# Performance work log

Measured on AMD Instinct MI355X. Metric: run time of the kernel, lower is better.

## Reference

```python
import jax, jax.numpy as jnp
import numpy as np

B, S, D, E = 4, 4096, 1024, 8

def setup_inputs() -> dict:
    key = jax.random.key(0)
    k1, k2, k3, k4, k5 = jax.random.split(key, 5)
    scale = 1.0 / np.sqrt(D)
    return {
        "x": jax.random.normal(k1, (B, S, D), dtype=jnp.float32),
        "Wg": jax.random.normal(k2, (D, D), dtype=jnp.float32) * scale,   # gate Linear(D, D)
        "bg": jnp.zeros((D,), dtype=jnp.float32),
        "We": jax.random.normal(k3, (E, D, D), dtype=jnp.float32) * scale,  # per-expert Linear(D, D)
        "be": jnp.zeros((E, D), dtype=jnp.float32),
    }

def reference(x, Wg, bg, We, be):
    # gating network: Linear + Softmax over last dim (size D, per the original module)
    probs = jax.nn.softmax(x @ Wg + bg, axis=-1)           # [B,S,D]
    idx = jnp.argmax(probs, axis=-1)                        # [B,S], values in [0, D)
    p = jnp.take_along_axis(probs, idx[..., None], axis=-1)[..., 0]  # top-1 gate prob
    e_idx = idx % We.shape[0]                               # map argmax to expert id
    # run every expert densely, then select routed expert per token (top-1 switch routing)
    h = jax.nn.relu(jnp.einsum('bsd,edf->besf', x, We) + be[None, :, None, :])  # [B,E,S,D]
    onehot = jax.nn.one_hot(e_idx, We.shape[0], dtype=x.dtype)                   # [B,S,E]
    out = jnp.einsum('besf,bse->bsf', h, onehot) * p[..., None]                  # [B,S,D]
    return out
```

## Files before the change

### kernel.cpp

```cpp
#include <hip/hip_runtime.h>
#include <stdint.h>
#include <stddef.h>

#define TOK    16384
#define DDIM   1024
#define NEXP   8
#define BMT    128
#define RB_MAX 136
#define MARGIN 2.5e-2f
#define AMBIG_CAP 4096
#define BK     64

typedef __bf16 bf16x8 __attribute__((ext_vector_type(8)));
typedef float  f32x4  __attribute__((ext_vector_type(4)));
typedef unsigned short u16x8 __attribute__((ext_vector_type(8)));

__device__ __forceinline__ unsigned short f2bf(float f) {
    unsigned int u = __float_as_uint(f);
    u += 0x7fff + ((u >> 16) & 1);
    return (unsigned short)(u >> 16);
}

__device__ __forceinline__ void gload_lds16(const void* g, void* l) {
    __builtin_amdgcn_global_load_lds(
        (const __attribute__((address_space(1))) unsigned int*)g,
        (__attribute__((address_space(3))) unsigned int*)l, 16, 0, 0);
}

__device__ __forceinline__ void seg_starts(const int* __restrict__ cnt, int* st) {
    int total = 0;
#pragma unroll
    for (int e = 0; e < NEXP; e++) {
        st[e] = total;
        total += ((cnt[e] + BMT - 1) / BMT) * BMT;
    }
    st[NEXP] = total;
}

__global__ __launch_bounds__(256) void cvt_x_init(
    const float* __restrict__ x, unsigned short* __restrict__ xbf,
    int* __restrict__ cnt, int* __restrict__ cursor,
    int* __restrict__ n_ambig, int* __restrict__ row_of_slot)
{
    if (blockIdx.x == 0) {
        for (int i = threadIdx.x; i < RB_MAX * BMT; i += 256) row_of_slot[i] = -1;
        if (threadIdx.x < NEXP) { cnt[threadIdx.x] = 0; cursor[threadIdx.x] = 0; }
        if (threadIdx.x == 0) *n_ambig = 0;
    }
    const size_t t = ((size_t)blockIdx.x * 256 + threadIdx.x) * 8;
    const float4 v0 = *(const float4*)(x + t);
    const float4 v1 = *(const float4*)(x + t + 4);
    const float vv[8] = {v0.x, v0.y, v0.z, v0.w, v1.x, v1.y, v1.z, v1.w};
    u16x8 hh;
#pragma unroll
    for (int j = 0; j < 8; j++) hh[j] = f2bf(vv[j]);
    *(u16x8*)(xbf + t) = hh;
}

__global__ __launch_bounds__(256) void transpose_mat(
    const float* __restrict__ src0, unsigned short* __restrict__ dst0)
{
    __shared__ float tile[32][33];
    const int e  = blockIdx.z;
    const int k0 = blockIdx.x * 32;
    const int n0 = blockIdx.y * 32;
    const int tx = threadIdx.x;
    const int ty = threadIdx.y;
    const float* src = src0 + (size_t)e * DDIM * DDIM;
    unsigned short* dst = dst0 + (size_t)e * DDIM * DDIM;
#pragma unroll
    for (int r = 0; r < 4; r++)
        tile[ty + r * 8][tx] = src[(size_t)(k0 + ty + r * 8) * DDIM + n0 + tx];
    __syncthreads();
#pragma unroll
    for (int r = 0; r < 4; r++)
        dst[(size_t)(n0 + ty + r * 8) * DDIM + k0 + tx] = f2bf(tile[tx][ty + r * 8]);
}

__global__ __launch_bounds__(256) void transpose_wg(
    const float* __restrict__ src, unsigned short* __restrict__ dstb,
    float* __restrict__ dstf)
{
    __shared__ float tile[32][33];
    const int k0 = blockIdx.x * 32;
    const int n0 = blockIdx.y * 32;
    const int tx = threadIdx.x;
    const int ty = threadIdx.y;
#pragma unroll
    for (int r = 0; r < 4; r++)
        tile[ty + r * 8][tx] = src[(size_t)(k0 + ty + r * 8) * DDIM + n0 + tx];
    __syncthreads();
#pragma unroll
    for (int r = 0; r < 4; r++) {
        const float v = tile[tx][ty + r * 8];
        const size_t o = (size_t)(n0 + ty + r * 8) * DDIM + k0 + tx;
        dstb[o] = f2bf(v);
        dstf[o] = v;
    }
}

__global__ __launch_bounds__(256) void gating_mfma(
    const unsigned short* __restrict__ xbf,
    const unsigned short* __restrict__ WgT,
    const float* __restrict__ bg, float* __restrict__ logits)
{
    __shared__ unsigned short Asm[128 * BK];
    __shared__ unsigned short Bsm[128 * BK];
    const int rb = blockIdx.x;
    const int nb = blockIdx.y;
    const int tid  = threadIdx.x;
    const int lane = tid & 63;
    const int wave = tid >> 6;
    const int q    = lane >> 4;
    const int m16  = lane & 15;
    const int wrow = (wave & 1) * 64;
    const int wcol = (wave >> 1) * 64;

    const unsigned short* Ag = xbf + (size_t)rb * 128 * DDIM;
    const unsigned short* Bg = WgT + (size_t)nb * 128 * DDIM;

    const unsigned short* pa[4];
    const unsigned short* pb[4];
#pragma unroll
    for (int i = 0; i < 4; i++) {
        const int idx = tid + i * 256;
        const int r = idx >> 3;
        const int c = idx & 7;
        const int g = (c ^ (r & 7)) * 8;
        pa[i] = Ag + (size_t)r * DDIM + g;
        pb[i] = Bg + (size_t)r * DDIM + g;
    }

    f32x4 acc[4][4];
#pragma unroll
    for (int i = 0; i < 4; i++)
#pragma unroll
        for (int j = 0; j < 4; j++) acc[i][j] = (f32x4){0.f, 0.f, 0.f, 0.f};

    for (int k0 = 0; k0 < DDIM; k0 += BK) {
#pragma unroll
        for (int i = 0; i < 4; i++) {
            gload_lds16(pa[i] + k0, &Asm[(tid + i * 256) * 8]);
            gload_lds16(pb[i] + k0, &Bsm[(tid + i * 256) * 8]);
        }
        __syncthreads();
#pragma unroll
        for (int s = 0; s < 2; s++) {
            const int cs = (((s << 2) + q) ^ (m16 & 7)) << 3;
            bf16x8 af[4], bfr[4];
#pragma unroll
            for (int i = 0; i < 4; i++)
                af[i] = *(const bf16x8*)&Asm[(wrow + i * 16 + m16) * BK + cs];
#pragma unroll
            for (int j = 0; j < 4; j++)
                bfr[j] = *(const bf16x8*)&Bsm[(wcol + j * 16 + m16) * BK + cs];
#pragma unroll
            for (int i = 0; i < 4; i++)
#pragma unroll
                for (int j = 0; j < 4; j++)
                    acc[i][j] = __builtin_amdgcn_mfma_f32_16x16x32_bf16(
                        af[i], bfr[j], acc[i][j], 0, 0, 0);
        }
        __syncthreads();
    }

    float bgv[4];
#pragma unroll
    for (int j = 0; j < 4; j++) bgv[j] = bg[nb * 128 + wcol + j * 16 + m16];
#pragma unroll
    for (int i = 0; i < 4; i++)
#pragma unroll
        for (int r = 0; r < 4; r++) {
            const int row = rb * 128 + wrow + i * 16 + q * 4 + r;
#pragma unroll
            for (int j = 0; j < 4; j++) {
                const int col = nb * 128 + wcol + j * 16 + m16;
                logits[(size_t)row * DDIM + col] = acc[i][j][r] + bgv[j];
            }
        }
}

__global__ __launch_bounds__(256) void row_stats(
    const float* __restrict__ logits, float* __restrict__ pout,
    int* __restrict__ eout, float* __restrict__ rmax_a, float* __restrict__ s_a,
    int* __restrict__ ambig, int* __restrict__ n_ambig)
{
    const int row  = blockIdx.x * 4 + (threadIdx.x >> 6);
    const int lane = threadIdx.x & 63;
    const float* L = logits + (size_t)row * DDIM;
    float vals[16];
#pragma unroll
    for (int i = 0; i < 4; i++)
        *(float4*)&vals[i * 4] = *(const float4*)&L[lane * 16 + i * 4];
    float m = vals[0]; int mi = lane * 16;
#pragma unroll
    for (int i = 1; i < 16; i++)
        if (vals[i] > m) { m = vals[i]; mi = lane * 16 + i; }
    for (int off = 32; off > 0; off >>= 1) {
        float ov = __shfl_down(m, off, 64);
        int   oi = __shfl_down(mi, off, 64);
        if (ov > m || (ov == m && oi < mi)) { m = ov; mi = oi; }
    }
    m  = __shfl(m, 0, 64);
    mi = __shfl(mi, 0, 64);
    float s = 0.f;
    int   c = 0;
#pragma unroll
    for (int i = 0; i < 16; i++) {
        s += expf(vals[i] - m);
        if (vals[i] >= m - MARGIN) c++;
    }
    for (int off = 32; off > 0; off >>= 1) {
        s += __shfl_xor(s, off, 64);
        c += __shfl_xor(c, off, 64);
    }
    if (lane == 0) {
        pout[row] = 1.0f / s;
        eout[row] = mi & (NEXP - 1);
        rmax_a[row] = m;
        s_a[row] = s;
        if (c > 1) {
            int k = atomicAdd(n_ambig, 1);
            if (k < AMBIG_CAP) ambig[k] = row;
        }
    }
}

__global__ __launch_bounds__(64) void fixup(
    const float* __restrict__ logits, const float* __restrict__ x,
    const float* __restrict__ WgTf, const float* __restrict__ bg,
    const float* __restrict__ rmax_a, const float* __restrict__ s_a,
    const int* __restrict__ ambig, const int* __restrict__ n_ambig,
    int* __restrict__ eout, float* __restrict__ pout)
{
    int n = *n_ambig; if (n > AMBIG_CAP) n = AMBIG_CAP;
    if ((int)blockIdx.x >= n) return;
    const int row  = ambig[blockIdx.x];
    const int lane = threadIdx.x;
    const float rmax = rmax_a[row];
    const float* L = logits + (size_t)row * DDIM;
    __shared__ int scnt;
    __shared__ int scol[32];
    if (lane == 0) scnt = 0;
    __syncthreads();
    for (int j = lane; j < DDIM; j += 64)
        if (L[j] >= rmax - MARGIN) {
            int k = atomicAdd(&scnt, 1);
            if (k < 32) scol[k] = j;
        }
    __syncthreads();
    int ncand = scnt < 32 ? scnt : 32;
    double bestv = -1e300; int bestc = DDIM;
    for (int cidx = 0; cidx < ncand; cidx++) {
        const int col = scol[cidx];
        const float* Wcol = WgTf + (size_t)col * DDIM;
        double s = 0.0;
        for (int k = lane; k < DDIM; k += 64)
            s += (double)x[(size_t)row * DDIM + k] * (double)Wcol[k];
        for (int off = 32; off > 0; off >>= 1) s += __shfl_down(s, off, 64);
        s = __shfl(s, 0, 64);
        s += (double)bg[col];
        if (s > bestv || (s == bestv && col < bestc)) { bestv = s; bestc = col; }
    }
    if (lane == 0) {
        eout[row] = bestc & (NEXP - 1);
        pout[row] = expf(L[bestc] - rmax) / s_a[row];
    }
}

__global__ __launch_bounds__(256) void histo(const int* __restrict__ eout,
                                             int* __restrict__ cnt)
{
    __shared__ int h[NEXP];
    if (threadIdx.x < NEXP) h[threadIdx.x] = 0;
    __syncthreads();
    const int t = blockIdx.x * 256 + threadIdx.x;
    if (t < TOK) atomicAdd(&h[eout[t]], 1);
    __syncthreads();
    if (threadIdx.x < NEXP) atomicAdd(&cnt[threadIdx.x], h[threadIdx.x]);
}

__global__ __launch_bounds__(256) void assign_slots(
    const int* __restrict__ eout, const int* __restrict__ cnt,
    int* __restrict__ cursor, int* __restrict__ row_of_slot)
{
    __shared__ int h[NEXP];
    __shared__ int base[NEXP];
    __shared__ int sstart[NEXP];
    const int tid = threadIdx.x;
    if (tid < NEXP) {
        h[tid] = 0;
        int st[NEXP + 1];
        seg_starts(cnt, st);
        sstart[tid] = st[tid];
    }
    __syncthreads();
    const int t = blockIdx.x * 256 + tid;
    int e = 0, lr = 0;
    if (t < TOK) {
        e = eout[t];
        lr = atomicAdd(&h[e], 1);
    }
    __syncthreads();
    if (tid < NEXP && h[tid] > 0)
        base[tid] = atomicAdd(&cursor[tid], h[tid]);
    __syncthreads();
    if (t < TOK)
        row_of_slot[sstart[e] + base[e] + lr] = t;
}

__global__ __launch_bounds__(256) void expert_gemm(
    const unsigned short* __restrict__ xbf, const unsigned short* __restrict__ WeT,
    const float* __restrict__ be, const float* __restrict__ p,
    const int* __restrict__ row_of_slot, const int* __restrict__ cnt,
    float* __restrict__ out)
{
    __shared__ unsigned short Asm[128 * BK];
    __shared__ unsigned short Bsm[128 * BK];
    __shared__ int rs[128];
    const int rb = blockIdx.x;
    const int nb = blockIdx.y;

    int st[NEXP + 1];
    seg_starts(cnt, st);
    const int s0 = rb * BMT;
    int e = -1;
#pragma unroll
    for (int ei = 0; ei < NEXP; ei++)
        if (s0 >= st[ei] && s0 < st[ei + 1]) e = ei;
    if (e < 0) return;

    const int tid  = threadIdx.x;
    const int lane = tid & 63;
    const int wave = tid >> 6;
    const int q    = lane >> 4;
    const int m16  = lane & 15;
    const int wrow = (wave & 1) * 64;
    const int wcol = (wave >> 1) * 64;

    if (tid < 128) rs[tid] = row_of_slot[rb * 128 + tid];
    __syncthreads();

    const unsigned short* Bglob = WeT + (size_t)e * DDIM * DDIM + (size_t)nb * 128 * DDIM;

    const unsigned short* pa[4];
    const unsigned short* pb[4];
#pragma unroll
    for (int i = 0; i < 4; i++) {
        const int idx = tid + i * 256;
        const int r = idx >> 3;
        const int c = idx & 7;
        const int g = (c ^ (r & 7)) * 8;
        int tr = rs[r]; if (tr < 0) tr = 0;
        pa[i] = xbf + (size_t)tr * DDIM + g;
        pb[i] = Bglob + (size_t)r * DDIM + g;
    }

    f32x4 acc[4][4];
#pragma unroll
    for (int i = 0; i < 4; i++)
#pragma unroll
        for (int j = 0; j < 4; j++) acc[i][j] = (f32x4){0.f, 0.f, 0.f, 0.f};

    for (int k0 = 0; k0 < DDIM; k0 += BK) {
#pragma unroll
        for (int i = 0; i < 4; i++) {
            gload_lds16(pa[i] + k0, &Asm[(tid + i * 256) * 8]);
            gload_lds16(pb[i] + k0, &Bsm[(tid + i * 256) * 8]);
        }
        __syncthreads();
#pragma unroll
        for (int s = 0; s < 2; s++) {
            const int cs = (((s << 2) + q) ^ (m16 & 7)) << 3;
            bf16x8 af[4], bfr[4];
#pragma unroll
            for (int i = 0; i < 4; i++)
                af[i] = *(const bf16x8*)&Asm[(wrow + i * 16 + m16) * BK + cs];
#pragma unroll
            for (int j = 0; j < 4; j++)
                bfr[j] = *(const bf16x8*)&Bsm[(wcol + j * 16 + m16) * BK + cs];
#pragma unroll
            for (int i = 0; i < 4; i++)
#pragma unroll
                for (int j = 0; j < 4; j++)
                    acc[i][j] = __builtin_amdgcn_mfma_f32_16x16x32_bf16(
                        af[i], bfr[j], acc[i][j], 0, 0, 0);
        }
        __syncthreads();
    }

    float bev[4];
#pragma unroll
    for (int j = 0; j < 4; j++) bev[j] = be[e * DDIM + nb * 128 + wcol + j * 16 + m16];
#pragma unroll
    for (int i = 0; i < 4; i++)
#pragma unroll
        for (int r = 0; r < 4; r++) {
            const int t = rs[wrow + i * 16 + q * 4 + r];
            if (t < 0) continue;
            const float pv = p[t];
#pragma unroll
            for (int j = 0; j < 4; j++) {
                const int n = nb * 128 + wcol + j * 16 + m16;
                float v = acc[i][j][r] + bev[j];
                v = v > 0.f ? v : 0.f;
                out[(size_t)t * DDIM + n] = v * pv;
            }
        }
}

extern "C" void kernel_launch(void* const* d_in, const int* in_sizes, int n_in,
                              void* d_out, int out_size, void* d_ws, size_t ws_size,
                              hipStream_t stream)
{
    const float* x  = (const float*)d_in[0];
    const float* Wg = (const float*)d_in[1];
    const float* bg = (const float*)d_in[2];
    const float* We = (const float*)d_in[3];
    const float* be = (const float*)d_in[4];
    float* out = (float*)d_out;

    char* ws = (char*)d_ws;
    float* logits = (float*)ws;                 ws += (size_t)TOK * DDIM * 4;
    unsigned short* WeT = (unsigned short*)ws;  ws += (size_t)NEXP * DDIM * DDIM * 2;
    unsigned short* WgT = (unsigned short*)ws;  ws += (size_t)DDIM * DDIM * 2;
    float* WgTf = (float*)ws;                   ws += (size_t)DDIM * DDIM * 4;
    unsigned short* xbf = (unsigned short*)ws;  ws += (size_t)TOK * DDIM * 2;
    float* p = (float*)ws;                      ws += (size_t)TOK * 4;
    int* e_arr = (int*)ws;                      ws += (size_t)TOK * 4;
    float* rmax_a = (float*)ws;                 ws += (size_t)TOK * 4;
    float* s_a = (float*)ws;                    ws += (size_t)TOK * 4;
    int* row_of_slot = (int*)ws;                ws += (size_t)RB_MAX * BMT * 4;
    int* cnt = (int*)ws;                        ws += NEXP * 4;
    int* cursor = (int*)ws;                     ws += NEXP * 4;
    int* ambig = (int*)ws;                      ws += AMBIG_CAP * 4;
    int* n_ambig = (int*)ws;                    ws += 4;

    cvt_x_init<<<TOK * DDIM / (256 * 8), 256, 0, stream>>>(
        x, xbf, cnt, cursor, n_ambig, row_of_slot);
    transpose_wg<<<dim3(32, 32), dim3(32, 8), 0, stream>>>(Wg, WgT, WgTf);
    transpose_mat<<<dim3(32, 32, NEXP), dim3(32, 8), 0, stream>>>(We, WeT);
    gating_mfma<<<dim3(TOK / 128, DDIM / 128), 256, 0, stream>>>(xbf, WgT, bg, logits);
    row_stats<<<TOK / 4, 256, 0, stream>>>(logits, p, e_arr, rmax_a, s_a, ambig, n_ambig);
    fixup<<<AMBIG_CAP, 64, 0, stream>>>(logits, x, WgTf, bg, rmax_a, s_a, ambig, n_ambig, e_arr, p);
    histo<<<TOK / 256, 256, 0, stream>>>(e_arr, cnt);
    assign_slots<<<TOK / 256, 256, 0, stream>>>(e_arr, cnt, cursor, row_of_slot);
    expert_gemm<<<dim3(RB_MAX, DDIM / 128), 256, 0, stream>>>(
        xbf, WeT, be, p, row_of_slot, cnt, out);
}
```

Measured before the change: 313.2 us.

## Fuse ambiguity fixup and histogram into row_stats; remap GEMM blocks per XCD

Folds the fp64 recheck of near-tie rows and the per-expert histogram into row_stats, which removes the fixup and histo launches along with the ambiguous-row list. Both GEMMs now use a 1D grid whose block index is remapped so that neighbouring row/column tiles land on the same XCD, aiming for better L2 reuse. The cost is that row_stats waves with ambiguous rows now run the fp64 dot products inline, which can stall their blocks.

After: 323.6 us. 3.3% more time.

```diff
diff --git a/kernel.cpp b/kernel.cpp
--- a/kernel.cpp
+++ b/kernel.cpp
@@ -8,7 +8,6 @@
 #define BMT    128
 #define RB_MAX 136
 #define MARGIN 2.5e-2f
-#define AMBIG_CAP 4096
 #define BK     64
 
 typedef __bf16 bf16x8 __attribute__((ext_vector_type(8)));
@@ -40,12 +39,11 @@
 __global__ __launch_bounds__(256) void cvt_x_init(
     const float* __restrict__ x, unsigned short* __restrict__ xbf,
     int* __restrict__ cnt, int* __restrict__ cursor,
-    int* __restrict__ n_ambig, int* __restrict__ row_of_slot)
+    int* __restrict__ row_of_slot)
 {
     if (blockIdx.x == 0) {
         for (int i = threadIdx.x; i < RB_MAX * BMT; i += 256) row_of_slot[i] = -1;
         if (threadIdx.x < NEXP) { cnt[threadIdx.x] = 0; cursor[threadIdx.x] = 0; }
-        if (threadIdx.x == 0) *n_ambig = 0;
     }
     const size_t t = ((size_t)blockIdx.x * 256 + threadIdx.x) * 8;
     const float4 v0 = *(const float4*)(x + t);
@@ -106,8 +104,13 @@
 {
     __shared__ unsigned short Asm[128 * BK];
     __shared__ unsigned short Bsm[128 * BK];
-    const int rb = blockIdx.x;
-    const int nb = blockIdx.y;
+    const int bid = blockIdx.x;
+    const int xcd = bid & 7;
+    const int seq = bid >> 3;
+    const int cl  = seq >> 6;
+    const int w   = seq & 63;
+    const int rb  = xcd * 16 + (w >> 2);
+    const int nb  = cl * 4 + (w & 3);
     const int tid  = threadIdx.x;
     const int lane = tid & 63;
     const int wave = tid >> 6;
@@ -181,12 +184,20 @@
 }
 
 __global__ __launch_bounds__(256) void row_stats(
-    const float* __restrict__ logits, float* __restrict__ pout,
-    int* __restrict__ eout, float* __restrict__ rmax_a, float* __restrict__ s_a,
-    int* __restrict__ ambig, int* __restrict__ n_ambig)
-{
-    const int row  = blockIdx.x * 4 + (threadIdx.x >> 6);
+    const float* __restrict__ logits, const float* __restrict__ x,
+    const float* __restrict__ WgTf, const float* __restrict__ bg,
+    float* __restrict__ pout, int* __restrict__ eout, int* __restrict__ cnt)
+{
+    __shared__ int   scnt[4];
+    __shared__ int   scol[4][32];
+    __shared__ float sval[4][32];
+    __shared__ int   hcnt[NEXP];
+    const int wv   = threadIdx.x >> 6;
+    const int row  = blockIdx.x * 4 + wv;
     const int lane = threadIdx.x & 63;
+    if (threadIdx.x < NEXP) hcnt[threadIdx.x] = 0;
+    __syncthreads();
+
     const float* L = logits + (size_t)row * DDIM;
     float vals[16];
 #pragma unroll
@@ -214,70 +225,45 @@
         s += __shfl_xor(s, off, 64);
         c += __shfl_xor(c, off, 64);
     }
+
+    int my_e; float my_p;
+    if (c > 1) {
+        if (lane == 0) scnt[wv] = 0;
+#pragma unroll
+        for (int i = 0; i < 16; i++)
+            if (vals[i] >= m - MARGIN) {
+                int k = atomicAdd(&scnt[wv], 1);
+                if (k < 32) { scol[wv][k] = lane * 16 + i; sval[wv][k] = vals[i]; }
+            }
+        int ncand = scnt[wv]; if (ncand > 32) ncand = 32;
+        double bestv = -1e300; int bestc = DDIM; float bestL = 0.f;
+        for (int cidx = 0; cidx < ncand; cidx++) {
+            const int col = scol[wv][cidx];
+            const float* Wcol = WgTf + (size_t)col * DDIM;
+            double sd = 0.0;
+            for (int k = lane; k < DDIM; k += 64)
+                sd += (double)x[(size_t)row * DDIM + k] * (double)Wcol[k];
+            for (int off = 32; off > 0; off >>= 1) sd += __shfl_down(sd, off, 64);
+            sd = __shfl(sd, 0, 64);
+            sd += (double)bg[col];
+            if (sd > bestv || (sd == bestv && col < bestc)) {
+                bestv = sd; bestc = col; bestL = sval[wv][cidx];
+            }
+        }
+        my_e = bestc & (NEXP - 1);
+        my_p = expf(bestL - m) / s;
+    } else {
+        my_e = mi & (NEXP - 1);
+        my_p = 1.0f / s;
+    }
     if (lane == 0) {
-        pout[row] = 1.0f / s;
-        eout[row] = mi & (NEXP - 1);
-        rmax_a[row] = m;
-        s_a[row] = s;
-        if (c > 1) {
-            int k = atomicAdd(n_ambig, 1);
-            if (k < AMBIG_CAP) ambig[k] = row;
-        }
-    }
-}
-
-__global__ __launch_bounds__(64) void fixup(
-    const float* __restrict__ logits, const float* __restrict__ x,
-    const float* __restrict__ WgTf, const float* __restrict__ bg,
-    const float* __restrict__ rmax_a, const float* __restrict__ s_a,
-    const int* __restrict__ ambig, const int* __restrict__ n_ambig,
-    int* __restrict__ eout, float* __restrict__ pout)
-{
-    int n = *n_ambig; if (n > AMBIG_CAP) n = AMBIG_CAP;
-    if ((int)blockIdx.x >= n) return;
-    const int row  = ambig[blockIdx.x];
-    const int lane = threadIdx.x;
-    const float rmax = rmax_a[row];
-    const float* L = logits + (size_t)row * DDIM;
-    __shared__ int scnt;
-    __shared__ int scol[32];
-    if (lane == 0) scnt = 0;
-    __syncthreads();
-    for (int j = lane; j < DDIM; j += 64)
-        if (L[j] >= rmax - MARGIN) {
-            int k = atomicAdd(&scnt, 1);
-            if (k < 32) scol[k] = j;
-        }
-    __syncthreads();
-    int ncand = scnt < 32 ? scnt : 32;
-    double bestv = -1e300; int bestc = DDIM;
-    for (int cidx = 0; cidx < ncand; cidx++) {
-        const int col = scol[cidx];
-        const float* Wcol = WgTf + (size_t)col * DDIM;
-        double s = 0.0;
-        for (int k = lane; k < DDIM; k += 64)
-            s += (double)x[(size_t)row * DDIM + k] * (double)Wcol[k];
-        for (int off = 32; off > 0; off >>= 1) s += __shfl_down(s, off, 64);
-        s = __shfl(s, 0, 64);
-        s += (double)bg[col];
-        if (s > bestv || (s == bestv && col < bestc)) { bestv = s; bestc = col; }
-    }
-    if (lane == 0) {
-        eout[row] = bestc & (NEXP - 1);
-        pout[row] = expf(L[bestc] - rmax) / s_a[row];
-    }
-}
-
-__global__ __launch_bounds__(256) void histo(const int* __restrict__ eout,
-                                             int* __restrict__ cnt)
-{
-    __shared__ int h[NEXP];
-    if (threadIdx.x < NEXP) h[threadIdx.x] = 0;
-    __syncthreads();
-    const int t = blockIdx.x * 256 + threadIdx.x;
-    if (t < TOK) atomicAdd(&h[eout[t]], 1);
-    __syncthreads();
-    if (threadIdx.x < NEXP) atomicAdd(&cnt[threadIdx.x], h[threadIdx.x]);
+        pout[row] = my_p;
+        eout[row] = my_e;
+        atomicAdd(&hcnt[my_e], 1);
+    }
+    __syncthreads();
+    if (threadIdx.x < NEXP && hcnt[threadIdx.x] > 0)
+        atomicAdd(&cnt[threadIdx.x], hcnt[threadIdx.x]);
 }
 
 __global__ __launch_bounds__(256) void assign_slots(
@@ -318,8 +304,13 @@
     __shared__ unsigned short Asm[128 * BK];
     __shared__ unsigned short Bsm[128 * BK];
     __shared__ int rs[128];
-    const int rb = blockIdx.x;
-    const int nb = blockIdx.y;
+    const int bid = blockIdx.x;
+    const int xcd = bid & 7;
+    const int seq = bid >> 3;
+    const int cl  = seq / 68;
+    const int w   = seq % 68;
+    const int rb  = xcd * 17 + (w >> 2);
+    const int nb  = cl * 4 + (w & 3);
 
     int st[NEXP + 1];
     seg_starts(cnt, st);
@@ -428,23 +419,17 @@
     unsigned short* xbf = (unsigned short*)ws;  ws += (size_t)TOK * DDIM * 2;
     float* p = (float*)ws;                      ws += (size_t)TOK * 4;
     int* e_arr = (int*)ws;                      ws += (size_t)TOK * 4;
-    float* rmax_a = (float*)ws;                 ws += (size_t)TOK * 4;
-    float* s_a = (float*)ws;                    ws += (size_t)TOK * 4;
     int* row_of_slot = (int*)ws;                ws += (size_t)RB_MAX * BMT * 4;
     int* cnt = (int*)ws;                        ws += NEXP * 4;
     int* cursor = (int*)ws;                     ws += NEXP * 4;
-    int* ambig = (int*)ws;                      ws += AMBIG_CAP * 4;
-    int* n_ambig = (int*)ws;                    ws += 4;
 
     cvt_x_init<<<TOK * DDIM / (256 * 8), 256, 0, stream>>>(
-        x, xbf, cnt, cursor, n_ambig, row_of_slot);
+        x, xbf, cnt, cursor, row_of_slot);
     transpose_wg<<<dim3(32, 32), dim3(32, 8), 0, stream>>>(Wg, WgT, WgTf);
     transpose_mat<<<dim3(32, 32, NEXP), dim3(32, 8), 0, stream>>>(We, WeT);
-    gating_mfma<<<dim3(TOK / 128, DDIM / 128), 256, 0, stream>>>(xbf, WgT, bg, logits);
-    row_stats<<<TOK / 4, 256, 0, stream>>>(logits, p, e_arr, rmax_a, s_a, ambig, n_ambig);
-    fixup<<<AMBIG_CAP, 64, 0, stream>>>(logits, x, WgTf, bg, rmax_a, s_a, ambig, n_ambig, e_arr, p);
-    histo<<<TOK / 256, 256, 0, stream>>>(e_arr, cnt);
+    gating_mfma<<<1024, 256, 0, stream>>>(xbf, WgT, bg, logits);
+    row_stats<<<TOK / 4, 256, 0, stream>>>(logits, x, WgTf, bg, p, e_arr, cnt);
     assign_slots<<<TOK / 256, 256, 0, stream>>>(e_arr, cnt, cursor, row_of_slot);
-    expert_gemm<<<dim3(RB_MAX, DDIM / 128), 256, 0, stream>>>(
+    expert_gemm<<<1088, 256, 0, stream>>>(
         xbf, WeT, be, p, row_of_slot, cnt, out);
 }
```
